# Kernel optimization log

Measured on AMD Instinct MI355X. Metric: run time of the kernel, lower is better.

The kernel has to match this reference:

```python
import jax, jax.numpy as jnp
import numpy as np

N_NODES = 100000
N_EDGES = 1600000
D_IN = 128
D_HID = 128
D_OUT = 40


def _linear_init(key, fan_in, fan_out):
    # torch nn.Linear default: U(-1/sqrt(fan_in), 1/sqrt(fan_in)) for W and b
    kw, kb = jax.random.split(key)
    bound = 1.0 / np.sqrt(fan_in)
    W = jax.random.uniform(kw, (fan_in, fan_out), jnp.float32, -bound, bound)
    b = jax.random.uniform(kb, (fan_out,), jnp.float32, -bound, bound)
    return W, b


def setup_inputs() -> dict:
    key = jax.random.key(0)
    ks = jax.random.split(key, 8)
    x = jax.random.normal(ks[0], (N_NODES, D_IN), jnp.float32)
    edges = jax.random.randint(ks[1], (2, N_EDGES), 0, N_NODES, jnp.int64)
    # layer 0: MLP(128 -> 128 -> 128)
    W1_0, b1_0 = _linear_init(ks[2], D_IN, D_HID)
    W2_0, b2_0 = _linear_init(ks[3], D_HID, D_HID)
    # layer 1: MLP(128 -> 128 -> 128)
    W1_1, b1_1 = _linear_init(ks[4], D_HID, D_HID)
    W2_1, b2_1 = _linear_init(ks[5], D_HID, D_HID)
    # layer 2: MLP(128 -> 128 -> 40)
    W1_2, b1_2 = _linear_init(ks[6], D_HID, D_HID)
    W2_2, b2_2 = _linear_init(ks[7], D_HID, D_OUT)
    eps = jnp.zeros(())  # GINConv train_eps=True initializes eps=0
    return {
        "x": x, "edges": edges,
        "W1_0": W1_0, "b1_0": b1_0, "W2_0": W2_0, "b2_0": b2_0, "eps_0": eps,
        "W1_1": W1_1, "b1_1": b1_1, "W2_1": W2_1, "b2_1": b2_1, "eps_1": eps,
        "W1_2": W1_2, "b1_2": b1_2, "W2_2": W2_2, "b2_2": b2_2, "eps_2": eps,
    }


def _gin_conv(x, src, dst, eps, W1, b1, W2, b2):
    # sum-aggregate neighbor features: out_i = MLP((1+eps)*x_i + sum_{j->i} x_j)
    aggr = jax.ops.segment_sum(x[src], dst, num_segments=x.shape[0])
    h = (1.0 + eps) * x + aggr
    h = jnp.maximum(h @ W1 + b1, 0.0)  # MLP layer 1 + ReLU
    return h @ W2 + b2                  # MLP layer 2


def reference(x, edges,
              W1_0, b1_0, W2_0, b2_0, eps_0,
              W1_1, b1_1, W2_1, b2_1, eps_1,
              W1_2, b1_2, W2_2, b2_2, eps_2):
    src, dst = edges[0], edges[1]
    # dropout is identity at inference (training=False)
    h = jax.nn.relu(_gin_conv(x, src, dst, eps_0, W1_0, b1_0, W2_0, b2_0))
    h = jax.nn.relu(_gin_conv(h, src, dst, eps_1, W1_1, b1_1, W2_1, b2_1))
    o = _gin_conv(h, src, dst, eps_2, W1_2, b1_2, W2_2, b2_2)
    return jax.nn.log_softmax(o, axis=1)
```

## Files before the change

kernel.cpp:

```cpp
#include <hip/hip_runtime.h>
#include <stdint.h>

typedef __attribute__((ext_vector_type(8))) short short8;
typedef __attribute__((ext_vector_type(4))) short short4v;
typedef __attribute__((ext_vector_type(4))) float float4v;

__device__ __forceinline__ float bf2f(unsigned short s) {
    union { unsigned int u; float f; } c; c.u = ((unsigned int)s) << 16; return c.f;
}
__device__ __forceinline__ unsigned short f2bf(float f) {
    union { float f; unsigned int u; } c; c.f = f;
    unsigned int x = c.u;
    unsigned int r = x + 0x7fffu + ((x >> 16) & 1u);
    return (unsigned short)(r >> 16);
}
__device__ __forceinline__ void unpack2(unsigned int u, float& lo, float& hi) {
    union { unsigned int uu; float ff; } a, b;
    a.uu = u << 16;
    b.uu = u & 0xffff0000u;
    lo = a.ff; hi = b.ff;
}


__global__ __launch_bounds__(512) void bs_scan(const int* __restrict__ bucketCnt,
                                               int* __restrict__ bucketBase,
                                               int* __restrict__ bucketCur,
                                               int* __restrict__ off, int M, int nE) {
    __shared__ int s[512];
    int t = threadIdx.x;
    int v = bucketCnt[t];
    s[t] = v;
    __syncthreads();
    for (int o = 1; o < 512; o <<= 1) {
        int x = (t >= o) ? s[t - o] : 0;
        __syncthreads();
        s[t] += x;
        __syncthreads();
    }
    bucketBase[t] = s[t] - v;
    bucketCur[t] = s[t] - v;
    if (t == 511) bucketBase[512] = s[511];
    if (t == 0) off[M] = nE;
}

__global__ __launch_bounds__(512) void bs_scatter(const int* __restrict__ src,
                                                  const int* __restrict__ dst, int nE,
                                                  int* __restrict__ bucketCur,
                                                  unsigned int* __restrict__ ebuf) {
    __shared__ int cnt[512];
    __shared__ int excl[512];
    __shared__ int chunk[512];
    __shared__ unsigned int buf[4096];
    __shared__ unsigned short bkt[4096];
    int t = threadIdx.x;
    cnt[t] = 0;
    __syncthreads();
    int base = blockIdx.x * 4096;
    int n = nE - base; if (n > 4096) n = 4096;
    unsigned int pk[8]; int bk[8]; int rk[8];
#pragma unroll
    for (int u = 0; u < 8; ++u) {
        int i = t + u * 512;
        if (i < n) {
            int e = base + i;
            int d = dst[e];
            int b = d >> 8;
            bk[u] = b;
            pk[u] = (unsigned int)src[e] | ((unsigned int)(d & 255) << 17);
            rk[u] = atomicAdd(&cnt[b], 1);
        } else bk[u] = -1;
    }
    __syncthreads();
    excl[t] = cnt[t];
    __syncthreads();
    for (int o = 1; o < 512; o <<= 1) {
        int x = (t >= o) ? excl[t - o] : 0;
        __syncthreads();
        excl[t] += x;
        __syncthreads();
    }
    int ex = excl[t] - cnt[t];
    __syncthreads();
    excl[t] = ex;
    if (cnt[t]) chunk[t] = atomicAdd(&bucketCur[t], cnt[t]);
    __syncthreads();
#pragma unroll
    for (int u = 0; u < 8; ++u) {
        if (bk[u] >= 0) {
            int lp = excl[bk[u]] + rk[u];
            buf[lp] = pk[u];
            bkt[lp] = (unsigned short)bk[u];
        }
    }
    __syncthreads();
    for (int i = t; i < n; i += 512) {
        int b = bkt[i];
        ebuf[chunk[b] + (i - excl[b])] = buf[i];
    }
}

__global__ __launch_bounds__(512) void bs_build(const unsigned int* __restrict__ ebuf,
                                                const int* __restrict__ bucketBase,
                                                int* __restrict__ off,
                                                int* __restrict__ esrc, int M) {
    __shared__ int cnt[256];
    __shared__ int excl[256];
    __shared__ int obuf[5120];
    int t = threadIdx.x, b = blockIdx.x;
    int base = bucketBase[b];
    int n = bucketBase[b + 1] - base;
    if (t < 256) cnt[t] = 0;
    __syncthreads();
    unsigned int pk[10]; int dl[10]; int rk[10];
#pragma unroll
    for (int u = 0; u < 10; ++u) {
        int i = t + u * 512;
        if (i < n) {
            unsigned int p = ebuf[base + i];
            pk[u] = p;
            int d = (p >> 17) & 255;
            dl[u] = d;
            rk[u] = atomicAdd(&cnt[d], 1);
        } else dl[u] = -1;
    }
    __syncthreads();
    if (t < 256) excl[t] = cnt[t];
    __syncthreads();
    for (int o = 1; o < 256; o <<= 1) {
        int x = (t < 256 && t >= o) ? excl[t - o] : 0;
        __syncthreads();
        if (t < 256) excl[t] += x;
        __syncthreads();
    }
    if (t < 256) {
        int ex = excl[t] - cnt[t];
        int node = b * 256 + t;
        if (node < M) off[node] = base + ex;
        excl[t] = ex;
    }
    __syncthreads();
#pragma unroll
    for (int u = 0; u < 10; ++u) {
        if (dl[u] >= 0) {
            int lp = excl[dl[u]] + rk[u];
            if (lp < 5120) obuf[lp] = (int)(pk[u] & 0x1FFFF);
        }
    }
    __syncthreads();
    for (int i = t; i < n; i += 512) esrc[base + i] = obuf[i];
}

struct Prep {
    const float* W[6];
    unsigned short* hi[6];
    const float4* xin;
    uint2* xout;
    int n4;
    int nxBlocks;
    const int* dst;
    int nE;
    int* bucketCnt;
};

__global__ __launch_bounds__(256) void k_prep(Prep p) {
    __shared__ int c[512];
    int b = blockIdx.x;
    int t = threadIdx.x;
    if (b < 344) {
        int mat = b >> 6;
        int rel = b - mat * 64;
        int NPAD = (mat == 5) ? 48 : 128;
        int N = (mat == 5) ? 40 : 128;
        int idx = rel * 256 + t;
        if (idx >= NPAD * 128) return;
        int n = idx >> 7, k = idx & 127;
        float w = (n < N) ? p.W[mat][k * N + n] : 0.f;
        p.hi[mat][idx] = f2bf(w);
    } else if (b < 344 + p.nxBlocks) {
        int i = (b - 344) * 256 + t;
        if (i >= p.n4) return;
        float4 v = p.xin[i];
        uint2 o;
        o.x = ((unsigned int)f2bf(v.y) << 16) | f2bf(v.x);
        o.y = ((unsigned int)f2bf(v.w) << 16) | f2bf(v.z);
        p.xout[i] = o;
    } else {
        for (int i = t; i < 512; i += 256) c[i] = 0;
        __syncthreads();
        int base = (b - 344 - p.nxBlocks) * 4096;
        for (int i = t; i < 4096; i += 256) {
            int e = base + i;
            if (e < p.nE) atomicAdd(&c[p.dst[e] >> 8], 1);
        }
        __syncthreads();
        for (int i = t; i < 512; i += 256)
            if (c[i]) atomicAdd(&p.bucketCnt[i], c[i]);
    }
}

__device__ __forceinline__ void acc8(uint4 v, float* s) {
    float a, b;
    unpack2(v.x, a, b); s[0] += a; s[1] += b;
    unpack2(v.y, a, b); s[2] += a; s[3] += b;
    unpack2(v.z, a, b); s[4] += a; s[5] += b;
    unpack2(v.w, a, b); s[6] += a; s[7] += b;
}

__global__ __launch_bounds__(256) void k_aggr(const uint4* __restrict__ Hin,
                                              const int* __restrict__ off,
                                              const int* __restrict__ esrc,
                                              const float* __restrict__ epsp,
                                              uint4* __restrict__ Ahi, int M) {
    int w = threadIdx.x >> 6, lane = threadIdx.x & 63;
    int li = lane & 15, q = lane >> 4;
    int node = blockIdx.x * 16 + w * 4 + q;
    if (node >= M) return;
    float ep = 1.0f + epsp[0];
    uint4 ow = Hin[node * 16 + li];
    float s[8] = {0.f, 0.f, 0.f, 0.f, 0.f, 0.f, 0.f, 0.f};
    int i = off[node], e = off[node + 1];
    int idx[8];
    if (i + 8 <= e) {
#pragma unroll
        for (int j = 0; j < 8; ++j) idx[j] = esrc[i + j];
    }
    while (i + 8 <= e) {
        uint4 v[8];
#pragma unroll
        for (int j = 0; j < 8; ++j) v[j] = Hin[idx[j] * 16 + li];
        int inext = i + 8;
        if (inext + 8 <= e) {
#pragma unroll
            for (int j = 0; j < 8; ++j) idx[j] = esrc[inext + j];
        }
#pragma unroll
        for (int j = 0; j < 8; ++j) acc8(v[j], s);
        i = inext;
    }
    if (i < e) {
        int last = e - 1;
        uint4 v[8];
#pragma unroll
        for (int j = 0; j < 8; ++j) {
            int k = i + j;
            int cl = k < last ? k : last;
            v[j] = Hin[esrc[cl] * 16 + li];
        }
#pragma unroll
        for (int j = 0; j < 8; ++j) {
            bool ok = (i + j) < e;
            uint4 u;
            u.x = ok ? v[j].x : 0u;
            u.y = ok ? v[j].y : 0u;
            u.z = ok ? v[j].z : 0u;
            u.w = ok ? v[j].w : 0u;
            acc8(u, s);
        }
    }
    float o[8];
    unpack2(ow.x, o[0], o[1]);
    unpack2(ow.y, o[2], o[3]);
    unpack2(ow.z, o[4], o[5]);
    unpack2(ow.w, o[6], o[7]);
#pragma unroll
    for (int k = 0; k < 8; ++k) s[k] = ep * o[k] + s[k];
    uint4 r;
    r.x = ((unsigned int)f2bf(s[1]) << 16) | f2bf(s[0]);
    r.y = ((unsigned int)f2bf(s[3]) << 16) | f2bf(s[2]);
    r.z = ((unsigned int)f2bf(s[5]) << 16) | f2bf(s[4]);
    r.w = ((unsigned int)f2bf(s[7]) << 16) | f2bf(s[6]);
    Ahi[node * 16 + li] = r;
}

template <int NT2, bool LOGITS>
__global__ __launch_bounds__(256, 3) void k_mlp(const unsigned short* __restrict__ AhiS,
                                                const unsigned short* __restrict__ W1h,
                                                const float* __restrict__ B1,
                                                const unsigned short* __restrict__ W2h,
                                                const float* __restrict__ B2,
                                                unsigned short* __restrict__ HOut,
                                                float* __restrict__ LOut, int M) {
    __shared__ short wbuf[128 * 136];
    int t = threadIdx.x, w = t >> 6, lane = t & 63;
    int lm = lane & 15, lg = lane >> 4;
    int rbase = blockIdx.x * 128;

    short8 xf2[2][4];
    bool act[2];
#pragma unroll
    for (int t2 = 0; t2 < 2; ++t2) {
        int r0 = rbase + t2 * 64 + w * 16;
        act[t2] = (r0 < M);
        if (act[t2]) {
            const short* Xp = (const short*)AhiS + (r0 + lm) * 128 + lg * 8;
#pragma unroll
            for (int kb = 0; kb < 4; ++kb) xf2[t2][kb] = *(const short8*)(Xp + kb * 32);
        } else {
#pragma unroll
            for (int kb = 0; kb < 4; ++kb) xf2[t2][kb] = (short8){0,0,0,0,0,0,0,0};
        }
    }
    constexpr int W2CH = (NT2 * 16 * 128) / 2048;
    short8 w1r[8], w2r[W2CH];
#pragma unroll
    for (int u = 0; u < 8; ++u) w1r[u] = *(const short8*)(W1h + t * 8 + u * 2048);
#pragma unroll
    for (int u = 0; u < W2CH; ++u) w2r[u] = *(const short8*)(W2h + t * 8 + u * 2048);

#pragma unroll
    for (int u = 0; u < 8; ++u) {
        int i = t * 8 + u * 2048;
        *(short8*)&wbuf[(i >> 7) * 136 + (i & 127)] = w1r[u];
    }
    __syncthreads();

    short4v h2[2][8];
#pragma unroll
    for (int t2 = 0; t2 < 2; ++t2) {
        float4v acc1[8];
#pragma unroll
        for (int nt = 0; nt < 8; ++nt) acc1[nt] = (float4v){0.f, 0.f, 0.f, 0.f};
#pragma unroll
        for (int nt = 0; nt < 8; ++nt) {
#pragma unroll
            for (int kb = 0; kb < 4; ++kb) {
                short8 wf = *(const short8*)&wbuf[(nt * 16 + lm) * 136 + kb * 32 + lg * 8];
                acc1[nt] = __builtin_amdgcn_mfma_f32_16x16x32_bf16(wf, xf2[t2][kb], acc1[nt], 0, 0, 0);
            }
        }
#pragma unroll
        for (int nt = 0; nt < 8; ++nt) {
            float4 b1 = *(const float4*)(B1 + nt * 16 + lg * 4);
            float v0 = acc1[nt][0] + b1.x; v0 = v0 > 0.f ? v0 : 0.f;
            float v1 = acc1[nt][1] + b1.y; v1 = v1 > 0.f ? v1 : 0.f;
            float v2 = acc1[nt][2] + b1.z; v2 = v2 > 0.f ? v2 : 0.f;
            float v3 = acc1[nt][3] + b1.w; v3 = v3 > 0.f ? v3 : 0.f;
            h2[t2][nt] = (short4v){(short)f2bf(v0), (short)f2bf(v1),
                                   (short)f2bf(v2), (short)f2bf(v3)};
        }
    }

    __syncthreads();
#pragma unroll
    for (int u = 0; u < W2CH; ++u) {
        int i = t * 8 + u * 2048;
        *(short8*)&wbuf[(i >> 7) * 136 + (i & 127)] = w2r[u];
    }
    __syncthreads();

    float4v acc2[2][NT2];
#pragma unroll
    for (int t2 = 0; t2 < 2; ++t2)
#pragma unroll
        for (int ot = 0; ot < NT2; ++ot) acc2[t2][ot] = (float4v){0.f, 0.f, 0.f, 0.f};
#pragma unroll
    for (int ot = 0; ot < NT2; ++ot) {
#pragma unroll
        for (int nt = 0; nt < 8; ++nt) {
            short4v wf = *(const short4v*)&wbuf[(ot * 16 + lm) * 136 + nt * 16 + lg * 4];
#pragma unroll
            for (int t2 = 0; t2 < 2; ++t2)
                acc2[t2][ot] = __builtin_amdgcn_mfma_f32_16x16x16bf16_1k(wf, h2[t2][nt],
                                                                         acc2[t2][ot], 0, 0, 0);
        }
    }

#pragma unroll
    for (int t2 = 0; t2 < 2; ++t2) {
        if (!act[t2]) continue;
        int row = rbase + t2 * 64 + w * 16 + lm;
        if (!LOGITS) {
#pragma unroll
            for (int ot = 0; ot < NT2; ++ot) {
                float4 b2 = *(const float4*)(B2 + ot * 16 + lg * 4);
                float v0 = acc2[t2][ot][0] + b2.x; v0 = v0 > 0.f ? v0 : 0.f;
                float v1 = acc2[t2][ot][1] + b2.y; v1 = v1 > 0.f ? v1 : 0.f;
                float v2 = acc2[t2][ot][2] + b2.z; v2 = v2 > 0.f ? v2 : 0.f;
                float v3 = acc2[t2][ot][3] + b2.w; v3 = v3 > 0.f ? v3 : 0.f;
                uint2 pk;
                pk.x = ((unsigned int)f2bf(v1) << 16) | f2bf(v0);
                pk.y = ((unsigned int)f2bf(v3) << 16) | f2bf(v2);
                *(uint2*)(HOut + row * 128 + ot * 16 + lg * 4) = pk;
            }
        } else {
            float vv[NT2][4];
#pragma unroll
            for (int ot = 0; ot < NT2; ++ot) {
                int ub = ot * 16 + lg * 4;
                bool valid = ub <= 36;
                float4 b2 = valid ? *(const float4*)(B2 + ub) : (float4){0.f, 0.f, 0.f, 0.f};
                vv[ot][0] = valid ? acc2[t2][ot][0] + b2.x : -1e30f;
                vv[ot][1] = valid ? acc2[t2][ot][1] + b2.y : -1e30f;
                vv[ot][2] = valid ? acc2[t2][ot][2] + b2.z : -1e30f;
                vv[ot][3] = valid ? acc2[t2][ot][3] + b2.w : -1e30f;
            }
            float m = -1e30f;
#pragma unroll
            for (int ot = 0; ot < NT2; ++ot)
#pragma unroll
                for (int r = 0; r < 4; ++r) m = fmaxf(m, vv[ot][r]);
            m = fmaxf(m, __shfl_xor(m, 16, 64));
            m = fmaxf(m, __shfl_xor(m, 32, 64));
            float s = 0.f;
#pragma unroll
            for (int ot = 0; ot < NT2; ++ot)
#pragma unroll
                for (int r = 0; r < 4; ++r)
                    s += (vv[ot][r] > -1e29f) ? expf(vv[ot][r] - m) : 0.f;
            s += __shfl_xor(s, 16, 64);
            s += __shfl_xor(s, 32, 64);
            float ls = m + logf(s);
#pragma unroll
            for (int ot = 0; ot < NT2; ++ot) {
                int ub = ot * 16 + lg * 4;
                if (ub <= 36) {
                    float4 outv = {vv[ot][0] - ls, vv[ot][1] - ls,
                                   vv[ot][2] - ls, vv[ot][3] - ls};
                    *(float4*)(LOut + row * 40 + ub) = outv;
                }
            }
        }
    }
}

extern "C" void kernel_launch(void* const* d_in, const int* in_sizes, int n_in,
                              void* d_out, int out_size, void* d_ws, size_t ws_size,
                              hipStream_t stream) {
    const float* x    = (const float*)d_in[0];
    const int*   edges = (const int*)d_in[1];
    const float* eps0 = (const float*)d_in[6];
    const float* eps1 = (const float*)d_in[11];
    const float* eps2 = (const float*)d_in[16];
    const float* B1[3] = {(const float*)d_in[3], (const float*)d_in[8], (const float*)d_in[13]};
    const float* B2[3] = {(const float*)d_in[5], (const float*)d_in[10], (const float*)d_in[15]};

    int M  = in_sizes[0] / 128;
    int nE = in_sizes[1] / 2;
    const int* e_src = edges;
    const int* e_dst = edges + nE;

    char* ws = (char*)d_ws;
    size_t o = 0;
    auto alloc = [&](size_t bytes) {
        size_t p = o;
        o = (o + bytes + 511) & ~(size_t)511;
        return ws + p;
    };
    int* bucketCnt  = (int*)alloc(512 * 4);
    int* bucketBase = (int*)alloc(513 * 4);
    int* bucketCur  = (int*)alloc(512 * 4);
    int* off  = (int*)alloc((size_t)(M + 1) * 4);
    int* esrc = (int*)alloc((size_t)nE * 4);
    unsigned int* ebuf = (unsigned int*)alloc((size_t)nE * 4);

    Prep pp;
    pp.W[0] = (const float*)d_in[2];  pp.W[1] = (const float*)d_in[4];
    pp.W[2] = (const float*)d_in[7];  pp.W[3] = (const float*)d_in[9];
    pp.W[4] = (const float*)d_in[12]; pp.W[5] = (const float*)d_in[14];
    for (int m = 0; m < 6; ++m) {
        int npad = (m == 5) ? 48 : 128;
        pp.hi[m] = (unsigned short*)alloc((size_t)npad * 128 * 2);
    }
    unsigned short* xb  = (unsigned short*)alloc((size_t)M * 128 * 2);
    unsigned short* Ahi = (unsigned short*)alloc((size_t)M * 128 * 2);
    unsigned short* Hb  = (unsigned short*)alloc((size_t)M * 128 * 2);
    pp.xin = (const float4*)x;
    pp.xout = (uint2*)xb;
    pp.n4 = M * 32;
    pp.nxBlocks = (pp.n4 + 255) / 256;
    pp.dst = e_dst;
    pp.nE = nE;
    pp.bucketCnt = bucketCnt;
    (void)ws_size; (void)n_in; (void)out_size;

    int nChunk = (nE + 4095) / 4096;
    int nBk = (M + 255) / 256;

    hipMemsetAsync(bucketCnt, 0, 512 * 4, stream);
    k_prep<<<344 + pp.nxBlocks + nChunk, 256, 0, stream>>>(pp);
    bs_scan<<<1, 512, 0, stream>>>(bucketCnt, bucketBase, bucketCur, off, M, nE);
    bs_scatter<<<nChunk, 512, 0, stream>>>(e_src, e_dst, nE, bucketCur, ebuf);
    bs_build<<<nBk, 512, 0, stream>>>(ebuf, bucketBase, off, esrc, M);

    int gA = (M + 15) / 16;
    int gG = (M + 127) / 128;

    k_aggr<<<gA, 256, 0, stream>>>((const uint4*)xb, off, esrc, eps0, (uint4*)Ahi, M);
    k_mlp<8, false><<<gG, 256, 0, stream>>>(Ahi, pp.hi[0], B1[0],
                                            pp.hi[1], B2[0], Hb, nullptr, M);
    k_aggr<<<gA, 256, 0, stream>>>((const uint4*)Hb, off, esrc, eps1, (uint4*)Ahi, M);
    k_mlp<8, false><<<gG, 256, 0, stream>>>(Ahi, pp.hi[2], B1[1],
                                            pp.hi[3], B2[1], Hb, nullptr, M);
    k_aggr<<<gA, 256, 0, stream>>>((const uint4*)Hb, off, esrc, eps2, (uint4*)Ahi, M);
    k_mlp<3, true><<<gG, 256, 0, stream>>>(Ahi, pp.hi[4], B1[2],
                                           pp.hi[5], B2[2], nullptr,
                                           (float*)d_out, M);
}
```

Before: 411.2 us.

## Fuse CSR build and GIN layers into cooperative persistent kernels with grid sync

Replaces the chain of about ten separate launches with two cooperative kernels. The first does weight and feature conversion, bucket counting, scan, scatter and CSR build, separated by grid-wide barriers. The second runs all three aggregate+MLP layers persistently with dynamic work counters, and the MLP now handles 256-row tiles with 512 threads. A probe launch decides whether cooperative launch is available and falls back to the old multi-kernel path otherwise. The aim is to remove launch gaps and tail effects, at the cost of grid-sync overhead and the limited occupancy a persistent grid allows.

```diff
diff --git a/kernel.cpp b/kernel.cpp
--- a/kernel.cpp
+++ b/kernel.cpp
@@ -1,13 +1,13 @@
 #include <hip/hip_runtime.h>
+#include <hip/hip_cooperative_groups.h>
 #include <stdint.h>
+
+namespace cg = cooperative_groups;
 
 typedef __attribute__((ext_vector_type(8))) short short8;
 typedef __attribute__((ext_vector_type(4))) short short4v;
 typedef __attribute__((ext_vector_type(4))) float float4v;
 
-__device__ __forceinline__ float bf2f(unsigned short s) {
-    union { unsigned int u; float f; } c; c.u = ((unsigned int)s) << 16; return c.f;
-}
 __device__ __forceinline__ unsigned short f2bf(float f) {
     union { float f; unsigned int u; } c; c.f = f;
     unsigned int x = c.u;
@@ -20,137 +20,480 @@
     b.uu = u & 0xffff0000u;
     lo = a.ff; hi = b.ff;
 }
-
-
-__global__ __launch_bounds__(512) void bs_scan(const int* __restrict__ bucketCnt,
-                                               int* __restrict__ bucketBase,
-                                               int* __restrict__ bucketCur,
-                                               int* __restrict__ off, int M, int nE) {
-    __shared__ int s[512];
-    int t = threadIdx.x;
-    int v = bucketCnt[t];
-    s[t] = v;
-    __syncthreads();
-    for (int o = 1; o < 512; o <<= 1) {
-        int x = (t >= o) ? s[t - o] : 0;
-        __syncthreads();
-        s[t] += x;
-        __syncthreads();
-    }
-    bucketBase[t] = s[t] - v;
-    bucketCur[t] = s[t] - v;
-    if (t == 511) bucketBase[512] = s[511];
-    if (t == 0) off[M] = nE;
-}
-
-__global__ __launch_bounds__(512) void bs_scatter(const int* __restrict__ src,
-                                                  const int* __restrict__ dst, int nE,
-                                                  int* __restrict__ bucketCur,
-                                                  unsigned int* __restrict__ ebuf) {
-    __shared__ int cnt[512];
-    __shared__ int excl[512];
-    __shared__ int chunk[512];
-    __shared__ unsigned int buf[4096];
-    __shared__ unsigned short bkt[4096];
-    int t = threadIdx.x;
-    cnt[t] = 0;
-    __syncthreads();
-    int base = blockIdx.x * 4096;
-    int n = nE - base; if (n > 4096) n = 4096;
-    unsigned int pk[8]; int bk[8]; int rk[8];
-#pragma unroll
-    for (int u = 0; u < 8; ++u) {
-        int i = t + u * 512;
-        if (i < n) {
-            int e = base + i;
-            int d = dst[e];
-            int b = d >> 8;
-            bk[u] = b;
-            pk[u] = (unsigned int)src[e] | ((unsigned int)(d & 255) << 17);
-            rk[u] = atomicAdd(&cnt[b], 1);
-        } else bk[u] = -1;
-    }
-    __syncthreads();
-    excl[t] = cnt[t];
-    __syncthreads();
-    for (int o = 1; o < 512; o <<= 1) {
-        int x = (t >= o) ? excl[t - o] : 0;
-        __syncthreads();
-        excl[t] += x;
-        __syncthreads();
-    }
-    int ex = excl[t] - cnt[t];
-    __syncthreads();
-    excl[t] = ex;
-    if (cnt[t]) chunk[t] = atomicAdd(&bucketCur[t], cnt[t]);
-    __syncthreads();
-#pragma unroll
-    for (int u = 0; u < 8; ++u) {
-        if (bk[u] >= 0) {
-            int lp = excl[bk[u]] + rk[u];
-            buf[lp] = pk[u];
-            bkt[lp] = (unsigned short)bk[u];
-        }
-    }
-    __syncthreads();
-    for (int i = t; i < n; i += 512) {
-        int b = bkt[i];
-        ebuf[chunk[b] + (i - excl[b])] = buf[i];
-    }
-}
-
-__global__ __launch_bounds__(512) void bs_build(const unsigned int* __restrict__ ebuf,
-                                                const int* __restrict__ bucketBase,
-                                                int* __restrict__ off,
-                                                int* __restrict__ esrc, int M) {
-    __shared__ int cnt[256];
-    __shared__ int excl[256];
-    __shared__ int obuf[5120];
-    int t = threadIdx.x, b = blockIdx.x;
-    int base = bucketBase[b];
-    int n = bucketBase[b + 1] - base;
-    if (t < 256) cnt[t] = 0;
-    __syncthreads();
-    unsigned int pk[10]; int dl[10]; int rk[10];
-#pragma unroll
-    for (int u = 0; u < 10; ++u) {
-        int i = t + u * 512;
-        if (i < n) {
-            unsigned int p = ebuf[base + i];
-            pk[u] = p;
-            int d = (p >> 17) & 255;
-            dl[u] = d;
-            rk[u] = atomicAdd(&cnt[d], 1);
-        } else dl[u] = -1;
-    }
-    __syncthreads();
-    if (t < 256) excl[t] = cnt[t];
-    __syncthreads();
-    for (int o = 1; o < 256; o <<= 1) {
-        int x = (t < 256 && t >= o) ? excl[t - o] : 0;
-        __syncthreads();
-        if (t < 256) excl[t] += x;
-        __syncthreads();
-    }
-    if (t < 256) {
-        int ex = excl[t] - cnt[t];
-        int node = b * 256 + t;
-        if (node < M) off[node] = base + ex;
-        excl[t] = ex;
-    }
-    __syncthreads();
-#pragma unroll
-    for (int u = 0; u < 10; ++u) {
-        if (dl[u] >= 0) {
-            int lp = excl[dl[u]] + rk[u];
-            if (lp < 5120) obuf[lp] = (int)(pk[u] & 0x1FFFF);
-        }
-    }
-    __syncthreads();
-    for (int i = t; i < n; i += 512) esrc[base + i] = obuf[i];
-}
-
-struct Prep {
+__device__ __forceinline__ void acc8(uint4 v, float* s) {
+    float a, b;
+    unpack2(v.x, a, b); s[0] += a; s[1] += b;
+    unpack2(v.y, a, b); s[2] += a; s[3] += b;
+    unpack2(v.z, a, b); s[4] += a; s[5] += b;
+    unpack2(v.w, a, b); s[6] += a; s[7] += b;
+}
+
+__device__ __forceinline__ void aggr_node(int node, int li,
+                                          const uint4* __restrict__ Hin,
+                                          const int* __restrict__ off,
+                                          const int* __restrict__ esrc,
+                                          float ep, uint4* __restrict__ Ahi) {
+    uint4 ow = Hin[node * 16 + li];
+    float s[8] = {0.f, 0.f, 0.f, 0.f, 0.f, 0.f, 0.f, 0.f};
+    int i = off[node], e = off[node + 1];
+    int idx[8];
+    if (i + 8 <= e) {
+#pragma unroll
+        for (int j = 0; j < 8; ++j) idx[j] = esrc[i + j];
+    }
+    while (i + 8 <= e) {
+        uint4 v[8];
+#pragma unroll
+        for (int j = 0; j < 8; ++j) v[j] = Hin[idx[j] * 16 + li];
+        int inext = i + 8;
+        if (inext + 8 <= e) {
+#pragma unroll
+            for (int j = 0; j < 8; ++j) idx[j] = esrc[inext + j];
+        }
+#pragma unroll
+        for (int j = 0; j < 8; ++j) acc8(v[j], s);
+        i = inext;
+    }
+    if (i < e) {
+        int last = e - 1;
+        uint4 v[8];
+#pragma unroll
+        for (int j = 0; j < 8; ++j) {
+            int k = i + j;
+            int cl = k < last ? k : last;
+            v[j] = Hin[esrc[cl] * 16 + li];
+        }
+#pragma unroll
+        for (int j = 0; j < 8; ++j) {
+            bool ok = (i + j) < e;
+            uint4 u2;
+            u2.x = ok ? v[j].x : 0u;
+            u2.y = ok ? v[j].y : 0u;
+            u2.z = ok ? v[j].z : 0u;
+            u2.w = ok ? v[j].w : 0u;
+            acc8(u2, s);
+        }
+    }
+    float o[8];
+    unpack2(ow.x, o[0], o[1]);
+    unpack2(ow.y, o[2], o[3]);
+    unpack2(ow.z, o[4], o[5]);
+    unpack2(ow.w, o[6], o[7]);
+#pragma unroll
+    for (int k = 0; k < 8; ++k) s[k] = ep * o[k] + s[k];
+    uint4 r;
+    r.x = ((unsigned int)f2bf(s[1]) << 16) | f2bf(s[0]);
+    r.y = ((unsigned int)f2bf(s[3]) << 16) | f2bf(s[2]);
+    r.z = ((unsigned int)f2bf(s[5]) << 16) | f2bf(s[4]);
+    r.w = ((unsigned int)f2bf(s[7]) << 16) | f2bf(s[6]);
+    Ahi[node * 16 + li] = r;
+}
+
+template <int NT2, bool LOGITS>
+__device__ void mlp_phase(short* wbuf,
+                          const unsigned short* __restrict__ AhiS,
+                          const unsigned short* __restrict__ W1h, const float* __restrict__ B1,
+                          const unsigned short* __restrict__ W2h, const float* __restrict__ B2,
+                          unsigned short* __restrict__ HOut, float* __restrict__ LOut, int M) {
+    int t = threadIdx.x, w = t >> 6, lane = t & 63;
+    int lm = lane & 15, lg = lane >> 4;
+    int h = w >> 2, wq = w & 3;
+    int nTP = (M + 255) / 256;
+    for (int tp = blockIdx.x; tp < nTP; tp += gridDim.x) {
+        __syncthreads();
+        int rbase = tp * 256 + h * 128;
+
+        short8 xf2[2][4];
+        bool act[2];
+#pragma unroll
+        for (int t2 = 0; t2 < 2; ++t2) {
+            int r0 = rbase + t2 * 64 + wq * 16;
+            act[t2] = (r0 < M);
+            if (act[t2]) {
+                const short* Xp = (const short*)AhiS + (r0 + lm) * 128 + lg * 8;
+#pragma unroll
+                for (int kb = 0; kb < 4; ++kb) xf2[t2][kb] = *(const short8*)(Xp + kb * 32);
+            } else {
+#pragma unroll
+                for (int kb = 0; kb < 4; ++kb) xf2[t2][kb] = (short8){0,0,0,0,0,0,0,0};
+            }
+        }
+        constexpr int WTOT2 = NT2 * 16 * 128;
+        constexpr int W2CH = (WTOT2 + 4095) / 4096;
+        short8 w1r[4], w2r[W2CH];
+#pragma unroll
+        for (int u = 0; u < 4; ++u) w1r[u] = *(const short8*)(W1h + t * 8 + u * 4096);
+#pragma unroll
+        for (int u = 0; u < W2CH; ++u) {
+            int i = t * 8 + u * 4096;
+            if (i < WTOT2) w2r[u] = *(const short8*)(W2h + i);
+        }
+
+#pragma unroll
+        for (int u = 0; u < 4; ++u) {
+            int i = t * 8 + u * 4096;
+            *(short8*)&wbuf[(i >> 7) * 136 + (i & 127)] = w1r[u];
+        }
+        __syncthreads();
+
+        short4v h2[2][8];
+#pragma unroll
+        for (int t2 = 0; t2 < 2; ++t2) {
+            float4v acc1[8];
+#pragma unroll
+            for (int nt = 0; nt < 8; ++nt) acc1[nt] = (float4v){0.f, 0.f, 0.f, 0.f};
+#pragma unroll
+            for (int nt = 0; nt < 8; ++nt) {
+#pragma unroll
+                for (int kb = 0; kb < 4; ++kb) {
+                    short8 wf = *(const short8*)&wbuf[(nt * 16 + lm) * 136 + kb * 32 + lg * 8];
+                    acc1[nt] = __builtin_amdgcn_mfma_f32_16x16x32_bf16(wf, xf2[t2][kb], acc1[nt], 0, 0, 0);
+                }
+            }
+#pragma unroll
+            for (int nt = 0; nt < 8; ++nt) {
+                float4 b1 = *(const float4*)(B1 + nt * 16 + lg * 4);
+                float v0 = acc1[nt][0] + b1.x; v0 = v0 > 0.f ? v0 : 0.f;
+                float v1 = acc1[nt][1] + b1.y; v1 = v1 > 0.f ? v1 : 0.f;
+                float v2 = acc1[nt][2] + b1.z; v2 = v2 > 0.f ? v2 : 0.f;
+                float v3 = acc1[nt][3] + b1.w; v3 = v3 > 0.f ? v3 : 0.f;
+                h2[t2][nt] = (short4v){(short)f2bf(v0), (short)f2bf(v1),
+                                       (short)f2bf(v2), (short)f2bf(v3)};
+            }
+        }
+
+        __syncthreads();
+#pragma unroll
+        for (int u = 0; u < W2CH; ++u) {
+            int i = t * 8 + u * 4096;
+            if (i < WTOT2) *(short8*)&wbuf[(i >> 7) * 136 + (i & 127)] = w2r[u];
+        }
+        __syncthreads();
+
+        float4v acc2[2][NT2];
+#pragma unroll
+        for (int t2 = 0; t2 < 2; ++t2)
+#pragma unroll
+            for (int ot = 0; ot < NT2; ++ot) acc2[t2][ot] = (float4v){0.f, 0.f, 0.f, 0.f};
+#pragma unroll
+        for (int ot = 0; ot < NT2; ++ot) {
+#pragma unroll
+            for (int nt = 0; nt < 8; ++nt) {
+                short4v wf = *(const short4v*)&wbuf[(ot * 16 + lm) * 136 + nt * 16 + lg * 4];
+#pragma unroll
+                for (int t2 = 0; t2 < 2; ++t2)
+                    acc2[t2][ot] = __builtin_amdgcn_mfma_f32_16x16x16bf16_1k(wf, h2[t2][nt],
+                                                                             acc2[t2][ot], 0, 0, 0);
+            }
+        }
+
+#pragma unroll
+        for (int t2 = 0; t2 < 2; ++t2) {
+            if (!act[t2]) continue;
+            int row = rbase + t2 * 64 + wq * 16 + lm;
+            if (!LOGITS) {
+#pragma unroll
+                for (int ot = 0; ot < NT2; ++ot) {
+                    float4 b2 = *(const float4*)(B2 + ot * 16 + lg * 4);
+                    float v0 = acc2[t2][ot][0] + b2.x; v0 = v0 > 0.f ? v0 : 0.f;
+                    float v1 = acc2[t2][ot][1] + b2.y; v1 = v1 > 0.f ? v1 : 0.f;
+                    float v2 = acc2[t2][ot][2] + b2.z; v2 = v2 > 0.f ? v2 : 0.f;
+                    float v3 = acc2[t2][ot][3] + b2.w; v3 = v3 > 0.f ? v3 : 0.f;
+                    uint2 pk;
+                    pk.x = ((unsigned int)f2bf(v1) << 16) | f2bf(v0);
+                    pk.y = ((unsigned int)f2bf(v3) << 16) | f2bf(v2);
+                    *(uint2*)(HOut + row * 128 + ot * 16 + lg * 4) = pk;
+                }
+            } else {
+                float vv[NT2][4];
+#pragma unroll
+                for (int ot = 0; ot < NT2; ++ot) {
+                    int ub = ot * 16 + lg * 4;
+                    bool valid = ub <= 36;
+                    float4 b2 = valid ? *(const float4*)(B2 + ub) : (float4){0.f, 0.f, 0.f, 0.f};
+                    vv[ot][0] = valid ? acc2[t2][ot][0] + b2.x : -1e30f;
+                    vv[ot][1] = valid ? acc2[t2][ot][1] + b2.y : -1e30f;
+                    vv[ot][2] = valid ? acc2[t2][ot][2] + b2.z : -1e30f;
+                    vv[ot][3] = valid ? acc2[t2][ot][3] + b2.w : -1e30f;
+                }
+                float m = -1e30f;
+#pragma unroll
+                for (int ot = 0; ot < NT2; ++ot)
+#pragma unroll
+                    for (int r = 0; r < 4; ++r) m = fmaxf(m, vv[ot][r]);
+                m = fmaxf(m, __shfl_xor(m, 16, 64));
+                m = fmaxf(m, __shfl_xor(m, 32, 64));
+                float s = 0.f;
+#pragma unroll
+                for (int ot = 0; ot < NT2; ++ot)
+#pragma unroll
+                    for (int r = 0; r < 4; ++r)
+                        s += (vv[ot][r] > -1e29f) ? expf(vv[ot][r] - m) : 0.f;
+                s += __shfl_xor(s, 16, 64);
+                s += __shfl_xor(s, 32, 64);
+                float ls = m + logf(s);
+#pragma unroll
+                for (int ot = 0; ot < NT2; ++ot) {
+                    int ub = ot * 16 + lg * 4;
+                    if (ub <= 36) {
+                        float4 outv = {vv[ot][0] - ls, vv[ot][1] - ls,
+                                       vv[ot][2] - ls, vv[ot][3] - ls};
+                        *(float4*)(LOut + row * 40 + ub) = outv;
+                    }
+                }
+            }
+        }
+    }
+}
+
+struct PrepCsrP {
+    const float* W[6];
+    unsigned short* hi[6];
+    const float4* xin;
+    uint2* xout;
+    int n4;
+    const int* esrc_in;
+    const int* edst_in;
+    int nE;
+    int* bucketCnt;
+    int* bucketBase;
+    int* bucketCur;
+    int* off;
+    unsigned int* ebuf;
+    int* esrc;
+    int M;
+    int nChunk;
+    int nBk;
+    int* aggrCtr;
+};
+
+#define GSYNC(g) do { __threadfence(); (g).sync(); __threadfence(); } while (0)
+
+__global__ __launch_bounds__(512, 4) void k_prepcsr(PrepCsrP p) {
+    cg::grid_group grid = cg::this_grid();
+    __shared__ char smem[30720];
+    int b = blockIdx.x, t = threadIdx.x, nb = gridDim.x;
+
+    if (b == 0) {
+        p.bucketCnt[t] = 0;
+        if (t < 3) p.aggrCtr[t] = 0;
+    }
+#pragma unroll
+    for (int mat = 0; mat < 6; ++mat) {
+        int NPAD = (mat == 5) ? 48 : 128;
+        int N = (mat == 5) ? 40 : 128;
+        int tot = NPAD * 128;
+        for (int i = b * 512 + t; i < tot; i += nb * 512) {
+            int n = i >> 7, k = i & 127;
+            float w = (n < N) ? p.W[mat][k * N + n] : 0.f;
+            p.hi[mat][i] = f2bf(w);
+        }
+    }
+    for (int i = b * 512 + t; i < p.n4; i += nb * 512) {
+        float4 v = p.xin[i];
+        uint2 o;
+        o.x = ((unsigned int)f2bf(v.y) << 16) | f2bf(v.x);
+        o.y = ((unsigned int)f2bf(v.w) << 16) | f2bf(v.z);
+        p.xout[i] = o;
+    }
+    GSYNC(grid);
+
+    {
+        int* c = (int*)smem;
+        for (int ch = b; ch < p.nChunk; ch += nb) {
+            c[t] = 0;
+            __syncthreads();
+            int base = ch * 4096;
+            for (int i = t; i < 4096; i += 512) {
+                int e = base + i;
+                if (e < p.nE) atomicAdd(&c[p.edst_in[e] >> 8], 1);
+            }
+            __syncthreads();
+            if (c[t]) atomicAdd(&p.bucketCnt[t], c[t]);
+            __syncthreads();
+        }
+    }
+    GSYNC(grid);
+
+    if (b == 0) {
+        int* s = (int*)smem;
+        int v = p.bucketCnt[t];
+        s[t] = v;
+        __syncthreads();
+        for (int o = 1; o < 512; o <<= 1) {
+            int x = (t >= o) ? s[t - o] : 0;
+            __syncthreads();
+            s[t] += x;
+            __syncthreads();
+        }
+        p.bucketBase[t] = s[t] - v;
+        p.bucketCur[t] = s[t] - v;
+        if (t == 511) p.bucketBase[512] = s[511];
+        if (t == 0) p.off[p.M] = p.nE;
+    }
+    GSYNC(grid);
+
+    {
+        int* cnt = (int*)smem;
+        int* excl = cnt + 512;
+        int* chunk = excl + 512;
+        unsigned int* buf = (unsigned int*)(chunk + 512);
+        unsigned short* bkt = (unsigned short*)(buf + 4096);
+        for (int ch = b; ch < p.nChunk; ch += nb) {
+            cnt[t] = 0;
+            __syncthreads();
+            int base = ch * 4096;
+            int n = p.nE - base; if (n > 4096) n = 4096;
+            unsigned int pk[8]; int bk[8]; int rk[8];
+#pragma unroll
+            for (int u = 0; u < 8; ++u) {
+                int i = t + u * 512;
+                if (i < n) {
+                    int e = base + i;
+                    int d = p.edst_in[e];
+                    int bb = d >> 8;
+                    bk[u] = bb;
+                    pk[u] = (unsigned int)p.esrc_in[e] | ((unsigned int)(d & 255) << 17);
+                    rk[u] = atomicAdd(&cnt[bb], 1);
+                } else bk[u] = -1;
+            }
+            __syncthreads();
+            excl[t] = cnt[t];
+            __syncthreads();
+            for (int o = 1; o < 512; o <<= 1) {
+                int x = (t >= o) ? excl[t - o] : 0;
+                __syncthreads();
+                excl[t] += x;
+                __syncthreads();
+            }
+            int ex = excl[t] - cnt[t];
+            __syncthreads();
+            excl[t] = ex;
+            if (cnt[t]) chunk[t] = atomicAdd(&p.bucketCur[t], cnt[t]);
+            __syncthreads();
+#pragma unroll
+            for (int u = 0; u < 8; ++u) {
+                if (bk[u] >= 0) {
+                    int lp = excl[bk[u]] + rk[u];
+                    buf[lp] = pk[u];
+                    bkt[lp] = (unsigned short)bk[u];
+                }
+            }
+            __syncthreads();
+            for (int i = t; i < n; i += 512) {
+                int bb = bkt[i];
+                p.ebuf[chunk[bb] + (i - excl[bb])] = buf[i];
+            }
+            __syncthreads();
+        }
+    }
+    GSYNC(grid);
+
+    {
+        int* cnt = (int*)smem;
+        int* excl = cnt + 256;
+        int* obuf = excl + 256;
+        for (int bb = b; bb < p.nBk; bb += nb) {
+            int base = p.bucketBase[bb];
+            int n = p.bucketBase[bb + 1] - base;
+            if (t < 256) cnt[t] = 0;
+            __syncthreads();
+            unsigned int pk[10]; int dl[10]; int rk[10];
+#pragma unroll
+            for (int u = 0; u < 10; ++u) {
+                int i = t + u * 512;
+                if (i < n) {
+                    unsigned int pw = p.ebuf[base + i];
+                    pk[u] = pw;
+                    int d = (pw >> 17) & 255;
+                    dl[u] = d;
+                    rk[u] = atomicAdd(&cnt[d], 1);
+                } else dl[u] = -1;
+            }
+            __syncthreads();
+            if (t < 256) excl[t] = cnt[t];
+            __syncthreads();
+            for (int o = 1; o < 256; o <<= 1) {
+                int x = (t < 256 && t >= o) ? excl[t - o] : 0;
+                __syncthreads();
+                if (t < 256) excl[t] += x;
+                __syncthreads();
+            }
+            if (t < 256) {
+                int ex = excl[t] - cnt[t];
+                int node = bb * 256 + t;
+                if (node < p.M) p.off[node] = base + ex;
+                excl[t] = ex;
+            }
+            __syncthreads();
+#pragma unroll
+            for (int u = 0; u < 10; ++u) {
+                if (dl[u] >= 0) {
+                    int lp = excl[dl[u]] + rk[u];
+                    if (lp < 5120) obuf[lp] = (int)(pk[u] & 0x1FFFF);
+                }
+            }
+            __syncthreads();
+            for (int i = t; i < n; i += 512) p.esrc[base + i] = obuf[i];
+            __syncthreads();
+        }
+    }
+}
+
+__device__ void aggr_queue(const uint4* __restrict__ Hin, const int* __restrict__ off,
+                           const int* __restrict__ esrc, const float* __restrict__ epsp,
+                           uint4* __restrict__ Ahi, int M, int* __restrict__ ctr) {
+    __shared__ int sg;
+    int w = threadIdx.x >> 6, lane = threadIdx.x & 63;
+    int li = lane & 15, q = lane >> 4;
+    float ep = 1.0f + epsp[0];
+    int nGrp = (M + 31) / 32;
+    while (true) {
+        __syncthreads();
+        if (threadIdx.x == 0) sg = atomicAdd(ctr, 1);
+        __syncthreads();
+        int g = sg;
+        if (g >= nGrp) break;
+        int node = g * 32 + w * 4 + q;
+        if (node < M) aggr_node(node, li, Hin, off, esrc, ep, Ahi);
+    }
+}
+
+struct LayersP {
+    const uint4* xb;
+    uint4* Ahi;
+    uint4* Hb;
+    const int* off;
+    const int* esrc;
+    const float* eps0; const float* eps1; const float* eps2;
+    const unsigned short* W1_0; const float* B1_0; const unsigned short* W2_0; const float* B2_0;
+    const unsigned short* W1_1; const float* B1_1; const unsigned short* W2_1; const float* B2_1;
+    const unsigned short* W1_2; const float* B1_2; const unsigned short* W2_2; const float* B2_2;
+    float* out;
+    int M;
+    int* aggrCtr;
+};
+
+__global__ __launch_bounds__(512, 4) void k_layers(LayersP L) {
+    cg::grid_group grid = cg::this_grid();
+    __shared__ short wbuf[128 * 136];
+    aggr_queue(L.xb, L.off, L.esrc, L.eps0, L.Ahi, L.M, L.aggrCtr + 0);
+    GSYNC(grid);
+    mlp_phase<8, false>(wbuf, (const unsigned short*)L.Ahi, L.W1_0, L.B1_0, L.W2_0, L.B2_0,
+                        (unsigned short*)L.Hb, nullptr, L.M);
+    GSYNC(grid);
+    aggr_queue((const uint4*)L.Hb, L.off, L.esrc, L.eps1, L.Ahi, L.M, L.aggrCtr + 1);
+    GSYNC(grid);
+    mlp_phase<8, false>(wbuf, (const unsigned short*)L.Ahi, L.W1_1, L.B1_1, L.W2_1, L.B2_1,
+                        (unsigned short*)L.xb, nullptr, L.M);
+    GSYNC(grid);
+    aggr_queue(L.xb, L.off, L.esrc, L.eps2, L.Ahi, L.M, L.aggrCtr + 2);
+    GSYNC(grid);
+    mlp_phase<3, true>(wbuf, (const unsigned short*)L.Ahi, L.W1_2, L.B1_2, L.W2_2, L.B2_2,
+                       nullptr, L.out, L.M);
+}
+
+struct FbPrep {
     const float* W[6];
     unsigned short* hi[6];
     const float4* xin;
@@ -162,7 +505,7 @@
     int* bucketCnt;
 };
 
-__global__ __launch_bounds__(256) void k_prep(Prep p) {
+__global__ __launch_bounds__(256) void fb_prep(FbPrep p) {
     __shared__ int c[512];
     int b = blockIdx.x;
     int t = threadIdx.x;
@@ -198,241 +541,165 @@
     }
 }
 
-__device__ __forceinline__ void acc8(uint4 v, float* s) {
-    float a, b;
-    unpack2(v.x, a, b); s[0] += a; s[1] += b;
-    unpack2(v.y, a, b); s[2] += a; s[3] += b;
-    unpack2(v.z, a, b); s[4] += a; s[5] += b;
-    unpack2(v.w, a, b); s[6] += a; s[7] += b;
-}
-
-__global__ __launch_bounds__(256) void k_aggr(const uint4* __restrict__ Hin,
-                                              const int* __restrict__ off,
-                                              const int* __restrict__ esrc,
-                                              const float* __restrict__ epsp,
-                                              uint4* __restrict__ Ahi, int M) {
+__global__ __launch_bounds__(512) void bs_scan(const int* __restrict__ bucketCnt,
+                                               int* __restrict__ bucketBase,
+                                               int* __restrict__ bucketCur,
+                                               int* __restrict__ off, int M, int nE) {
+    __shared__ int s[512];
+    int t = threadIdx.x;
+    int v = bucketCnt[t];
+    s[t] = v;
+    __syncthreads();
+    for (int o = 1; o < 512; o <<= 1) {
+        int x = (t >= o) ? s[t - o] : 0;
+        __syncthreads();
+        s[t] += x;
+        __syncthreads();
+    }
+    bucketBase[t] = s[t] - v;
+    bucketCur[t] = s[t] - v;
+    if (t == 511) bucketBase[512] = s[511];
+    if (t == 0) off[M] = nE;
+}
+
+__global__ __launch_bounds__(512) void bs_scatter(const int* __restrict__ src,
+                                                  const int* __restrict__ dst, int nE,
+                                                  int* __restrict__ bucketCur,
+                                                  unsigned int* __restrict__ ebuf) {
+    __shared__ int cnt[512];
+    __shared__ int excl[512];
+    __shared__ int chunk[512];
+    __shared__ unsigned int buf[4096];
+    __shared__ unsigned short bkt[4096];
+    int t = threadIdx.x;
+    cnt[t] = 0;
+    __syncthreads();
+    int base = blockIdx.x * 4096;
+    int n = nE - base; if (n > 4096) n = 4096;
+    unsigned int pk[8]; int bk[8]; int rk[8];
+#pragma unroll
+    for (int u = 0; u < 8; ++u) {
+        int i = t + u * 512;
+        if (i < n) {
+            int e = base + i;
+            int d = dst[e];
+            int b = d >> 8;
+            bk[u] = b;
+            pk[u] = (unsigned int)src[e] | ((unsigned int)(d & 255) << 17);
+            rk[u] = atomicAdd(&cnt[b], 1);
+        } else bk[u] = -1;
+    }
+    __syncthreads();
+    excl[t] = cnt[t];
+    __syncthreads();
+    for (int o = 1; o < 512; o <<= 1) {
+        int x = (t >= o) ? excl[t - o] : 0;
+        __syncthreads();
+        excl[t] += x;
+        __syncthreads();
+    }
+    int ex = excl[t] - cnt[t];
+    __syncthreads();
+    excl[t] = ex;
+    if (cnt[t]) chunk[t] = atomicAdd(&bucketCur[t], cnt[t]);
+    __syncthreads();
+#pragma unroll
+    for (int u = 0; u < 8; ++u) {
+        if (bk[u] >= 0) {
+            int lp = excl[bk[u]] + rk[u];
+            buf[lp] = pk[u];
+            bkt[lp] = (unsigned short)bk[u];
+        }
+    }
+    __syncthreads();
+    for (int i = t; i < n; i += 512) {
+        int b = bkt[i];
+        ebuf[chunk[b] + (i - excl[b])] = buf[i];
+    }
+}
+
+__global__ __launch_bounds__(512) void bs_build(const unsigned int* __restrict__ ebuf,
+                                                const int* __restrict__ bucketBase,
+                                                int* __restrict__ off,
+                                                int* __restrict__ esrc, int M) {
+    __shared__ int cnt[256];
+    __shared__ int excl[256];
+    __shared__ int obuf[5120];
+    int t = threadIdx.x, b = blockIdx.x;
+    int base = bucketBase[b];
+    int n = bucketBase[b + 1] - base;
+    if (t < 256) cnt[t] = 0;
+    __syncthreads();
+    unsigned int pk[10]; int dl[10]; int rk[10];
+#pragma unroll
+    for (int u = 0; u < 10; ++u) {
+        int i = t + u * 512;
+        if (i < n) {
+            unsigned int p = ebuf[base + i];
+            pk[u] = p;
+            int d = (p >> 17) & 255;
+            dl[u] = d;
+            rk[u] = atomicAdd(&cnt[d], 1);
+        } else dl[u] = -1;
+    }
+    __syncthreads();
+    if (t < 256) excl[t] = cnt[t];
+    __syncthreads();
+    for (int o = 1; o < 256; o <<= 1) {
+        int x = (t < 256 && t >= o) ? excl[t - o] : 0;
+        __syncthreads();
+        if (t < 256) excl[t] += x;
+        __syncthreads();
+    }
+    if (t < 256) {
+        int ex = excl[t] - cnt[t];
+        int node = b * 256 + t;
+        if (node < M) off[node] = base + ex;
+        excl[t] = ex;
+    }
+    __syncthreads();
+#pragma unroll
+    for (int u = 0; u < 10; ++u) {
+        if (dl[u] >= 0) {
+            int lp = excl[dl[u]] + rk[u];
+            if (lp < 5120) obuf[lp] = (int)(pk[u] & 0x1FFFF);
+        }
+    }
+    __syncthreads();
+    for (int i = t; i < n; i += 512) esrc[base + i] = obuf[i];
+}
+
+__global__ __launch_bounds__(256) void fb_aggr(const uint4* __restrict__ Hin,
+                                               const int* __restrict__ off,
+                                               const int* __restrict__ esrc,
+                                               const float* __restrict__ epsp,
+                                               uint4* __restrict__ Ahi, int M) {
     int w = threadIdx.x >> 6, lane = threadIdx.x & 63;
     int li = lane & 15, q = lane >> 4;
     int node = blockIdx.x * 16 + w * 4 + q;
     if (node >= M) return;
-    float ep = 1.0f + epsp[0];
-    uint4 ow = Hin[node * 16 + li];
-    float s[8] = {0.f, 0.f, 0.f, 0.f, 0.f, 0.f, 0.f, 0.f};
-    int i = off[node], e = off[node + 1];
-    int idx[8];
-    if (i + 8 <= e) {
-#pragma unroll
-        for (int j = 0; j < 8; ++j) idx[j] = esrc[i + j];
-    }
-    while (i + 8 <= e) {
-        uint4 v[8];
-#pragma unroll
-        for (int j = 0; j < 8; ++j) v[j] = Hin[idx[j] * 16 + li];
-        int inext = i + 8;
-        if (inext + 8 <= e) {
-#pragma unroll
-            for (int j = 0; j < 8; ++j) idx[j] = esrc[inext + j];
-        }
-#pragma unroll
-        for (int j = 0; j < 8; ++j) acc8(v[j], s);
-        i = inext;
-    }
-    if (i < e) {
-        int last = e - 1;
-        uint4 v[8];
-#pragma unroll
-        for (int j = 0; j < 8; ++j) {
-            int k = i + j;
-            int cl = k < last ? k : last;
-            v[j] = Hin[esrc[cl] * 16 + li];
-        }
-#pragma unroll
-        for (int j = 0; j < 8; ++j) {
-            bool ok = (i + j) < e;
-            uint4 u;
-            u.x = ok ? v[j].x : 0u;
-            u.y = ok ? v[j].y : 0u;
-            u.z = ok ? v[j].z : 0u;
-            u.w = ok ? v[j].w : 0u;
-            acc8(u, s);
-        }
-    }
-    float o[8];
-    unpack2(ow.x, o[0], o[1]);
-    unpack2(ow.y, o[2], o[3]);
-    unpack2(ow.z, o[4], o[5]);
-    unpack2(ow.w, o[6], o[7]);
-#pragma unroll
-    for (int k = 0; k < 8; ++k) s[k] = ep * o[k] + s[k];
-    uint4 r;
-    r.x = ((unsigned int)f2bf(s[1]) << 16) | f2bf(s[0]);
-    r.y = ((unsigned int)f2bf(s[3]) << 16) | f2bf(s[2]);
-    r.z = ((unsigned int)f2bf(s[5]) << 16) | f2bf(s[4]);
-    r.w = ((unsigned int)f2bf(s[7]) << 16) | f2bf(s[6]);
-    Ahi[node * 16 + li] = r;
+    aggr_node(node, li, Hin, off, esrc, 1.0f + epsp[0], Ahi);
 }
 
 template <int NT2, bool LOGITS>
-__global__ __launch_bounds__(256, 3) void k_mlp(const unsigned short* __restrict__ AhiS,
-                                                const unsigned short* __restrict__ W1h,
-                                                const float* __restrict__ B1,
-                                                const unsigned short* __restrict__ W2h,
-                                                const float* __restrict__ B2,
-                                                unsigned short* __restrict__ HOut,
-                                                float* __restrict__ LOut, int M) {
+__global__ __launch_bounds__(512, 4) void fb_mlp(const unsigned short* __restrict__ AhiS,
+                                                 const unsigned short* __restrict__ W1h,
+                                                 const float* __restrict__ B1,
+                                                 const unsigned short* __restrict__ W2h,
+                                                 const float* __restrict__ B2,
+                                                 unsigned short* __restrict__ HOut,
+                                                 float* __restrict__ LOut, int M) {
     __shared__ short wbuf[128 * 136];
-    int t = threadIdx.x, w = t >> 6, lane = t & 63;
-    int lm = lane & 15, lg = lane >> 4;
-    int rbase = blockIdx.x * 128;
-
-    short8 xf2[2][4];
-    bool act[2];
-#pragma unroll
-    for (int t2 = 0; t2 < 2; ++t2) {
-        int r0 = rbase + t2 * 64 + w * 16;
-        act[t2] = (r0 < M);
-        if (act[t2]) {
-            const short* Xp = (const short*)AhiS + (r0 + lm) * 128 + lg * 8;
-#pragma unroll
-            for (int kb = 0; kb < 4; ++kb) xf2[t2][kb] = *(const short8*)(Xp + kb * 32);
-        } else {
-#pragma unroll
-            for (int kb = 0; kb < 4; ++kb) xf2[t2][kb] = (short8){0,0,0,0,0,0,0,0};
-        }
-    }
-    constexpr int W2CH = (NT2 * 16 * 128) / 2048;
-    short8 w1r[8], w2r[W2CH];
-#pragma unroll
-    for (int u = 0; u < 8; ++u) w1r[u] = *(const short8*)(W1h + t * 8 + u * 2048);
-#pragma unroll
-    for (int u = 0; u < W2CH; ++u) w2r[u] = *(const short8*)(W2h + t * 8 + u * 2048);
-
-#pragma unroll
-    for (int u = 0; u < 8; ++u) {
-        int i = t * 8 + u * 2048;
-        *(short8*)&wbuf[(i >> 7) * 136 + (i & 127)] = w1r[u];
-    }
-    __syncthreads();
-
-    short4v h2[2][8];
-#pragma unroll
-    for (int t2 = 0; t2 < 2; ++t2) {
-        float4v acc1[8];
-#pragma unroll
-        for (int nt = 0; nt < 8; ++nt) acc1[nt] = (float4v){0.f, 0.f, 0.f, 0.f};
-#pragma unroll
-        for (int nt = 0; nt < 8; ++nt) {
-#pragma unroll
-            for (int kb = 0; kb < 4; ++kb) {
-                short8 wf = *(const short8*)&wbuf[(nt * 16 + lm) * 136 + kb * 32 + lg * 8];
-                acc1[nt] = __builtin_amdgcn_mfma_f32_16x16x32_bf16(wf, xf2[t2][kb], acc1[nt], 0, 0, 0);
-            }
-        }
-#pragma unroll
-        for (int nt = 0; nt < 8; ++nt) {
-            float4 b1 = *(const float4*)(B1 + nt * 16 + lg * 4);
-            float v0 = acc1[nt][0] + b1.x; v0 = v0 > 0.f ? v0 : 0.f;
-            float v1 = acc1[nt][1] + b1.y; v1 = v1 > 0.f ? v1 : 0.f;
-            float v2 = acc1[nt][2] + b1.z; v2 = v2 > 0.f ? v2 : 0.f;
-            float v3 = acc1[nt][3] + b1.w; v3 = v3 > 0.f ? v3 : 0.f;
-            h2[t2][nt] = (short4v){(short)f2bf(v0), (short)f2bf(v1),
-                                   (short)f2bf(v2), (short)f2bf(v3)};
-        }
-    }
-
-    __syncthreads();
-#pragma unroll
-    for (int u = 0; u < W2CH; ++u) {
-        int i = t * 8 + u * 2048;
-        *(short8*)&wbuf[(i >> 7) * 136 + (i & 127)] = w2r[u];
-    }
-    __syncthreads();
-
-    float4v acc2[2][NT2];
-#pragma unroll
-    for (int t2 = 0; t2 < 2; ++t2)
-#pragma unroll
-        for (int ot = 0; ot < NT2; ++ot) acc2[t2][ot] = (float4v){0.f, 0.f, 0.f, 0.f};
-#pragma unroll
-    for (int ot = 0; ot < NT2; ++ot) {
-#pragma unroll
-        for (int nt = 0; nt < 8; ++nt) {
-            short4v wf = *(const short4v*)&wbuf[(ot * 16 + lm) * 136 + nt * 16 + lg * 4];
-#pragma unroll
-            for (int t2 = 0; t2 < 2; ++t2)
-                acc2[t2][ot] = __builtin_amdgcn_mfma_f32_16x16x16bf16_1k(wf, h2[t2][nt],
-                                                                         acc2[t2][ot], 0, 0, 0);
-        }
-    }
-
-#pragma unroll
-    for (int t2 = 0; t2 < 2; ++t2) {
-        if (!act[t2]) continue;
-        int row = rbase + t2 * 64 + w * 16 + lm;
-        if (!LOGITS) {
-#pragma unroll
-            for (int ot = 0; ot < NT2; ++ot) {
-                float4 b2 = *(const float4*)(B2 + ot * 16 + lg * 4);
-                float v0 = acc2[t2][ot][0] + b2.x; v0 = v0 > 0.f ? v0 : 0.f;
-                float v1 = acc2[t2][ot][1] + b2.y; v1 = v1 > 0.f ? v1 : 0.f;
-                float v2 = acc2[t2][ot][2] + b2.z; v2 = v2 > 0.f ? v2 : 0.f;
-                float v3 = acc2[t2][ot][3] + b2.w; v3 = v3 > 0.f ? v3 : 0.f;
-                uint2 pk;
-                pk.x = ((unsigned int)f2bf(v1) << 16) | f2bf(v0);
-                pk.y = ((unsigned int)f2bf(v3) << 16) | f2bf(v2);
-                *(uint2*)(HOut + row * 128 + ot * 16 + lg * 4) = pk;
-            }
-        } else {
-            float vv[NT2][4];
-#pragma unroll
-            for (int ot = 0; ot < NT2; ++ot) {
-                int ub = ot * 16 + lg * 4;
-                bool valid = ub <= 36;
-                float4 b2 = valid ? *(const float4*)(B2 + ub) : (float4){0.f, 0.f, 0.f, 0.f};
-                vv[ot][0] = valid ? acc2[t2][ot][0] + b2.x : -1e30f;
-                vv[ot][1] = valid ? acc2[t2][ot][1] + b2.y : -1e30f;
-                vv[ot][2] = valid ? acc2[t2][ot][2] + b2.z : -1e30f;
-                vv[ot][3] = valid ? acc2[t2][ot][3] + b2.w : -1e30f;
-            }
-            float m = -1e30f;
-#pragma unroll
-            for (int ot = 0; ot < NT2; ++ot)
-#pragma unroll
-                for (int r = 0; r < 4; ++r) m = fmaxf(m, vv[ot][r]);
-            m = fmaxf(m, __shfl_xor(m, 16, 64));
-            m = fmaxf(m, __shfl_xor(m, 32, 64));
-            float s = 0.f;
-#pragma unroll
-            for (int ot = 0; ot < NT2; ++ot)
-#pragma unroll
-                for (int r = 0; r < 4; ++r)
-                    s += (vv[ot][r] > -1e29f) ? expf(vv[ot][r] - m) : 0.f;
-            s += __shfl_xor(s, 16, 64);
-            s += __shfl_xor(s, 32, 64);
-            float ls = m + logf(s);
-#pragma unroll
-            for (int ot = 0; ot < NT2; ++ot) {
-                int ub = ot * 16 + lg * 4;
-                if (ub <= 36) {
-                    float4 outv = {vv[ot][0] - ls, vv[ot][1] - ls,
-                                   vv[ot][2] - ls, vv[ot][3] - ls};
-                    *(float4*)(LOut + row * 40 + ub) = outv;
-                }
-            }
-        }
-    }
-}
+    mlp_phase<NT2, LOGITS>(wbuf, AhiS, W1h, B1, W2h, B2, HOut, LOut, M);
+}
+
+__global__ void k_probe(int x) { (void)x; }
 
 extern "C" void kernel_launch(void* const* d_in, const int* in_sizes, int n_in,
                               void* d_out, int out_size, void* d_ws, size_t ws_size,
                               hipStream_t stream) {
     const float* x    = (const float*)d_in[0];
     const int*   edges = (const int*)d_in[1];
-    const float* eps0 = (const float*)d_in[6];
-    const float* eps1 = (const float*)d_in[11];
-    const float* eps2 = (const float*)d_in[16];
-    const float* B1[3] = {(const float*)d_in[3], (const float*)d_in[8], (const float*)d_in[13]};
-    const float* B2[3] = {(const float*)d_in[5], (const float*)d_in[10], (const float*)d_in[15]};
 
     int M  = in_sizes[0] / 128;
     int nE = in_sizes[1] / 2;
@@ -449,50 +716,114 @@
     int* bucketCnt  = (int*)alloc(512 * 4);
     int* bucketBase = (int*)alloc(513 * 4);
     int* bucketCur  = (int*)alloc(512 * 4);
+    int* aggrCtr    = (int*)alloc(3 * 4);
     int* off  = (int*)alloc((size_t)(M + 1) * 4);
     int* esrc = (int*)alloc((size_t)nE * 4);
     unsigned int* ebuf = (unsigned int*)alloc((size_t)nE * 4);
 
-    Prep pp;
-    pp.W[0] = (const float*)d_in[2];  pp.W[1] = (const float*)d_in[4];
-    pp.W[2] = (const float*)d_in[7];  pp.W[3] = (const float*)d_in[9];
-    pp.W[4] = (const float*)d_in[12]; pp.W[5] = (const float*)d_in[14];
+    PrepCsrP pc;
+    pc.W[0] = (const float*)d_in[2];  pc.W[1] = (const float*)d_in[4];
+    pc.W[2] = (const float*)d_in[7];  pc.W[3] = (const float*)d_in[9];
+    pc.W[4] = (const float*)d_in[12]; pc.W[5] = (const float*)d_in[14];
     for (int m = 0; m < 6; ++m) {
         int npad = (m == 5) ? 48 : 128;
-        pp.hi[m] = (unsigned short*)alloc((size_t)npad * 128 * 2);
+        pc.hi[m] = (unsigned short*)alloc((size_t)npad * 128 * 2);
     }
     unsigned short* xb  = (unsigned short*)alloc((size_t)M * 128 * 2);
     unsigned short* Ahi = (unsigned short*)alloc((size_t)M * 128 * 2);
     unsigned short* Hb  = (unsigned short*)alloc((size_t)M * 128 * 2);
-    pp.xin = (const float4*)x;
-    pp.xout = (uint2*)xb;
-    pp.n4 = M * 32;
-    pp.nxBlocks = (pp.n4 + 255) / 256;
-    pp.dst = e_dst;
-    pp.nE = nE;
-    pp.bucketCnt = bucketCnt;
+    pc.xin = (const float4*)x;
+    pc.xout = (uint2*)xb;
+    pc.n4 = M * 32;
+    pc.esrc_in = e_src;
+    pc.edst_in = e_dst;
+    pc.nE = nE;
+    pc.bucketCnt = bucketCnt;
+    pc.bucketBase = bucketBase;
+    pc.bucketCur = bucketCur;
+    pc.off = off;
+    pc.ebuf = ebuf;
+    pc.esrc = esrc;
+    pc.M = M;
+    pc.nChunk = (nE + 4095) / 4096;
+    pc.nBk = (M + 255) / 256;
+    pc.aggrCtr = aggrCtr;
     (void)ws_size; (void)n_in; (void)out_size;
 
-    int nChunk = (nE + 4095) / 4096;
-    int nBk = (M + 255) / 256;
-
-    hipMemsetAsync(bucketCnt, 0, 512 * 4, stream);
-    k_prep<<<344 + pp.nxBlocks + nChunk, 256, 0, stream>>>(pp);
-    bs_scan<<<1, 512, 0, stream>>>(bucketCnt, bucketBase, bucketCur, off, M, nE);
-    bs_scatter<<<nChunk, 512, 0, stream>>>(e_src, e_dst, nE, bucketCur, ebuf);
-    bs_build<<<nBk, 512, 0, stream>>>(ebuf, bucketBase, off, esrc, M);
-
-    int gA = (M + 15) / 16;
-    int gG = (M + 127) / 128;
-
-    k_aggr<<<gA, 256, 0, stream>>>((const uint4*)xb, off, esrc, eps0, (uint4*)Ahi, M);
-    k_mlp<8, false><<<gG, 256, 0, stream>>>(Ahi, pp.hi[0], B1[0],
-                                            pp.hi[1], B2[0], Hb, nullptr, M);
-    k_aggr<<<gA, 256, 0, stream>>>((const uint4*)Hb, off, esrc, eps1, (uint4*)Ahi, M);
-    k_mlp<8, false><<<gG, 256, 0, stream>>>(Ahi, pp.hi[2], B1[1],
-                                            pp.hi[3], B2[1], Hb, nullptr, M);
-    k_aggr<<<gA, 256, 0, stream>>>((const uint4*)Hb, off, esrc, eps2, (uint4*)Ahi, M);
-    k_mlp<3, true><<<gG, 256, 0, stream>>>(Ahi, pp.hi[4], B1[2],
-                                           pp.hi[5], B2[2], nullptr,
-                                           (float*)d_out, M);
-}
+    LayersP Ls;
+    Ls.xb = (const uint4*)xb;
+    Ls.Ahi = (uint4*)Ahi;
+    Ls.Hb = (uint4*)Hb;
+    Ls.off = off;
+    Ls.esrc = esrc;
+    Ls.eps0 = (const float*)d_in[6];
+    Ls.eps1 = (const float*)d_in[11];
+    Ls.eps2 = (const float*)d_in[16];
+    Ls.W1_0 = pc.hi[0]; Ls.B1_0 = (const float*)d_in[3];
+    Ls.W2_0 = pc.hi[1]; Ls.B2_0 = (const float*)d_in[5];
+    Ls.W1_1 = pc.hi[2]; Ls.B1_1 = (const float*)d_in[8];
+    Ls.W2_1 = pc.hi[3]; Ls.B2_1 = (const float*)d_in[10];
+    Ls.W1_2 = pc.hi[4]; Ls.B1_2 = (const float*)d_in[13];
+    Ls.W2_2 = pc.hi[5]; Ls.B2_2 = (const float*)d_in[15];
+    Ls.out = (float*)d_out;
+    Ls.M = M;
+    Ls.aggrCtr = aggrCtr;
+
+    static int g_coop = -1;
+    if (g_coop < 0) {
+        g_coop = 0;
+        hipStream_t ps;
+        if (hipStreamCreateWithFlags(&ps, hipStreamNonBlocking) == hipSuccess) {
+            int zero = 0;
+            void* pa[] = { &zero };
+            if (hipLaunchCooperativeKernel((const void*)k_probe, dim3(2), dim3(64),
+                                           pa, 0, ps) == hipSuccess)
+                g_coop = 1;
+        }
+    }
+
+    bool done = false;
+    if (g_coop == 1) {
+        void* a1[] = { &pc };
+        void* a2[] = { &Ls };
+        hipError_t e1 = hipLaunchCooperativeKernel((const void*)k_prepcsr,
+                                                   dim3(pc.nChunk), dim3(512), a1, 0, stream);
+        hipError_t e2 = hipSuccess;
+        if (e1 == hipSuccess)
+            e2 = hipLaunchCooperativeKernel((const void*)k_layers,
+                                            dim3(512), dim3(512), a2, 0, stream);
+        if (e1 == hipSuccess && e2 == hipSuccess) done = true;
+        else g_coop = 0;
+    }
+
+    if (!done) {
+        FbPrep fp;
+        for (int m = 0; m < 6; ++m) { fp.W[m] = pc.W[m]; fp.hi[m] = pc.hi[m]; }
+        fp.xin = pc.xin;
+        fp.xout = pc.xout;
+        fp.n4 = pc.n4;
+        fp.nxBlocks = (pc.n4 + 255) / 256;
+        fp.dst = e_dst;
+        fp.nE = nE;
+        fp.bucketCnt = bucketCnt;
+
+        int nChunk = pc.nChunk, nBk = pc.nBk;
+        hipMemsetAsync(bucketCnt, 0, 512 * 4, stream);
+        fb_prep<<<344 + fp.nxBlocks + nChunk, 256, 0, stream>>>(fp);
+        bs_scan<<<1, 512, 0, stream>>>(bucketCnt, bucketBase, bucketCur, off, M, nE);
+        bs_scatter<<<nChunk, 512, 0, stream>>>(e_src, e_dst, nE, bucketCur, ebuf);
+        bs_build<<<nBk, 512, 0, stream>>>(ebuf, bucketBase, off, esrc, M);
+
+        int gA = (M + 15) / 16;
+        int nTP = (M + 255) / 256;
+        fb_aggr<<<gA, 256, 0, stream>>>((const uint4*)xb, off, esrc, Ls.eps0, (uint4*)Ahi, M);
+        fb_mlp<8, false><<<nTP, 512, 0, stream>>>((const unsigned short*)Ahi, Ls.W1_0, Ls.B1_0,
+                                                  Ls.W2_0, Ls.B2_0, Hb, nullptr, M);
+        fb_aggr<<<gA, 256, 0, stream>>>((const uint4*)Hb, off, esrc, Ls.eps1, (uint4*)Ahi, M);
+        fb_mlp<8, false><<<nTP, 512, 0, stream>>>((const unsigned short*)Ahi, Ls.W1_1, Ls.B1_1,
+                                                  Ls.W2_1, Ls.B2_1, xb, nullptr, M);
+        fb_aggr<<<gA, 256, 0, stream>>>((const uint4*)xb, off, esrc, Ls.eps2, (uint4*)Ahi, M);
+        fb_mlp<3, true><<<nTP, 512, 0, stream>>>((const unsigned short*)Ahi, Ls.W1_2, Ls.B1_2,
+                                                 Ls.W2_2, Ls.B2_2, nullptr, (float*)d_out, M);
+    }
+}
```

After: 629.4 us. +53.0%, slower.
